# Optimization experiments

Hardware: AMD Instinct MI355X
Metric: run time of the kernel (lower is better)

## Reference

```python
import jax, jax.numpy as jnp
import numpy as np
from jax import lax

K = 3
PAD = 1
STRIDE = 1


def setup_inputs() -> dict:
    key = jax.random.key(0)
    k1, k2, k3 = jax.random.split(key, 3)
    B, Cin, Cout, H, W = 4, 64, 64, 128, 128
    x = jax.random.normal(k1, (B, Cin, H, W), dtype=jnp.float32)
    # offset-generating conv weight: [2*K*K, Cin, K, K]
    w_offset = jax.random.normal(k2, (2 * K * K, Cin, K, K), dtype=jnp.float32) * 0.05
    # deformable conv weight: [Cout, Cin, K, K]
    w_deform = jax.random.normal(k3, (Cout, Cin, K, K), dtype=jnp.float32) * 0.05
    return {"x": x, "w_offset": w_offset, "w_deform": w_deform}


def _bilinear_sample_one(img, ys, xs):
    # img: [C, H, W]; ys, xs: [K2, Ho, Wo] float sampling coords
    H, W = img.shape[1], img.shape[2]
    y0 = jnp.floor(ys)
    x0 = jnp.floor(xs)
    wy = ys - y0  # frac weights, [K2, Ho, Wo]
    wx = xs - x0

    def gather(yi, xi):
        valid = (yi >= 0) & (yi <= H - 1) & (xi >= 0) & (xi <= W - 1)
        yc = jnp.clip(yi, 0, H - 1).astype(jnp.int32)
        xc = jnp.clip(xi, 0, W - 1).astype(jnp.int32)
        # img[:, yc, xc] -> [C, K2, Ho, Wo]; zero outside (torchvision zero-pad)
        return img[:, yc, xc] * valid[None].astype(img.dtype)

    v00 = gather(y0, x0)
    v01 = gather(y0, x0 + 1)
    v10 = gather(y0 + 1, x0)
    v11 = gather(y0 + 1, x0 + 1)
    w00 = ((1 - wy) * (1 - wx))[None]
    w01 = ((1 - wy) * wx)[None]
    w10 = (wy * (1 - wx))[None]
    w11 = (wy * wx)[None]
    return v00 * w00 + v01 * w01 + v10 * w10 + v11 * w11  # [C, K2, Ho, Wo]


def reference(x, w_offset, w_deform):
    B, Cin, H, W = x.shape
    Cout = w_deform.shape[0]
    K2 = K * K
    # 1) plain conv to produce offsets: [B, 2*K2, H, W]
    offset = lax.conv_general_dilated(
        x, w_offset, window_strides=(STRIDE, STRIDE),
        padding=((PAD, PAD), (PAD, PAD)),
        dimension_numbers=("NCHW", "OIHW", "NCHW"))
    Ho, Wo = offset.shape[2], offset.shape[3]
    # torchvision ordering: channel 2*k = dy, 2*k+1 = dx, taps row-major
    off = offset.reshape(B, K2, 2, Ho, Wo)
    dy, dx = off[:, :, 0], off[:, :, 1]  # [B, K2, Ho, Wo]
    # 2) base sampling grid per kernel tap
    kk = jnp.arange(K2)
    ki = (kk // K).astype(jnp.float32)  # tap row
    kj = (kk % K).astype(jnp.float32)   # tap col
    base_y = (jnp.arange(Ho, dtype=jnp.float32) * STRIDE - PAD)[None, :] + ki[:, None]  # [K2, Ho]
    base_x = (jnp.arange(Wo, dtype=jnp.float32) * STRIDE - PAD)[None, :] + kj[:, None]  # [K2, Wo]
    ys = base_y[None, :, :, None] + dy  # [B, K2, Ho, Wo]
    xs = base_x[None, :, None, :] + dx
    # 3) deformable bilinear gather: [B, Cin, K2, Ho, Wo]
    sampled = jax.vmap(_bilinear_sample_one)(x, ys, xs)
    # 4) weighted accumulation (the conv contraction)
    out = jnp.einsum("ock,bckhw->bohw", w_deform.reshape(Cout, Cin, K2), sampled)
    return out
```

## Files before the change

### kernel.cpp

```cpp
#include <hip/hip_runtime.h>


#define BATCH 4
#define CIN   64
#define COUT  64
#define HH    128
#define WW    128
#define HWPIX (HH*WW)

typedef __attribute__((ext_vector_type(8))) short short8;
typedef __attribute__((ext_vector_type(4))) float floatx4;

__device__ __forceinline__ unsigned short f2bf(float f) {
  unsigned int u = __float_as_uint(f);
  unsigned int r = u + 0x7fffu + ((u >> 16) & 1u);
  return (unsigned short)(r >> 16);
}
__device__ __forceinline__ float bf2f(unsigned short h) { return __uint_as_float(((unsigned int)h) << 16); }
__device__ __forceinline__ float lo16f(unsigned int u) { return __uint_as_float(u << 16); }
__device__ __forceinline__ float hi16f(unsigned int u) { return __uint_as_float(u & 0xffff0000u); }

__device__ __forceinline__ unsigned int bilin2(unsigned int u00, unsigned int u01,
                                               unsigned int u10, unsigned int u11,
                                               float w00, float w01, float w10, float w11) {
  float lo = w00 * lo16f(u00) + w01 * lo16f(u01) + w10 * lo16f(u10) + w11 * lo16f(u11);
  float hi = w00 * hi16f(u00) + w01 * hi16f(u01) + w10 * hi16f(u10) + w11 * hi16f(u11);
  return (unsigned int)f2bf(lo) | ((unsigned int)f2bf(hi) << 16);
}

__global__ __launch_bounds__(256) void pre_kernel(const float* __restrict__ x,
                                                  const float* __restrict__ wo,
                                                  const float* __restrict__ wd,
                                                  unsigned short* __restrict__ xThi,
                                                  unsigned short* __restrict__ xTlo,
                                                  unsigned short* __restrict__ wdA,
                                                  unsigned short* __restrict__ woAhi,
                                                  unsigned short* __restrict__ woAlo) {
  int tid = threadIdx.x;
  if (blockIdx.x < 4096) {
    __shared__ float tile[32][33];
    int t = blockIdx.x;
    int b = t >> 10, rem = t & 1023;
    int c0 = (rem >> 9) * 32, p0 = (rem & 511) * 32;
    int tx = tid & 31, ty = tid >> 5;
    const float* xb = x + (size_t)b * CIN * HWPIX;
    size_t boff = (size_t)b * HWPIX * CIN;
#pragma unroll
    for (int i = 0; i < 4; i++)
      tile[ty + i * 8][tx] = xb[(size_t)(c0 + ty + i * 8) * HWPIX + p0 + tx];
    __syncthreads();
#pragma unroll
    for (int i = 0; i < 2; i++) {
      int tt = tid + i * 256;
      int row = tt >> 4;
      int cp = tt & 15;
      float v0 = tile[cp * 2][row], v1 = tile[cp * 2 + 1][row];
      unsigned short h0 = f2bf(v0), h1 = f2bf(v1);
      unsigned short l0 = f2bf(v0 - bf2f(h0)), l1 = f2bf(v1 - bf2f(h1));
      size_t o = boff + (size_t)(p0 + row) * CIN + c0 + cp * 2;
      *(ushort2*)&xThi[o] = make_ushort2(h0, h1);
      *(ushort2*)&xTlo[o] = make_ushort2(l0, l1);
    }
  } else {
    int t = (blockIdx.x - 4096) * 256 + tid;
    if (t < 36864) {
      int j = t & 7, lane = (t >> 3) & 63, ct = (t >> 9) & 3, kc = (t >> 11) & 1, kk = t >> 12;
      int cout = ct * 16 + (lane & 15);
      int cin  = kc * 32 + (lane >> 4) * 8 + j;
      wdA[t] = f2bf(wd[(size_t)(cout * CIN + cin) * 9 + kk]);
    }
    int t2 = t - 36864;
    if (t2 >= 0 && t2 < 18432) {
      int j = t2 & 7, lane = (t2 >> 3) & 63, ct = (t2 >> 9) & 1, kc = (t2 >> 10) & 1, kk = t2 >> 11;
      int cout = ct * 16 + (lane & 15);
      int cin  = kc * 32 + (lane >> 4) * 8 + j;
      float v = (cout < 18) ? wo[(size_t)(cout * CIN + cin) * 9 + kk] : 0.f;
      unsigned short h = f2bf(v);
      woAhi[t2] = h;
      woAlo[t2] = f2bf(v - bf2f(h));
    }
  }
}

__global__ __launch_bounds__(256) void fused_dcn_kernel(const unsigned short* __restrict__ xThi,
                                                        const unsigned short* __restrict__ xTlo,
                                                        const unsigned short* __restrict__ woAhi,
                                                        const unsigned short* __restrict__ woAlo,
                                                        const unsigned short* __restrict__ wdA,
                                                        float* __restrict__ out) {
  __shared__ unsigned short sBhi[4096];
  __shared__ unsigned short sBlo[4096];
  __shared__ float offL[18 * 64];

  int tid = threadIdx.x;
  int hw = blockIdx.x;
  int bid = (hw & 7) * 128 + (hw >> 3);
  int b = bid >> 8, r = bid & 255, y = r >> 1, x0 = (r & 1) << 6;

  int p1 = tid >> 2, si = tid & 3;
  int lane = tid & 63, w = tid >> 6;

  const unsigned short* xhib = xThi + (size_t)b * HWPIX * CIN;
  const unsigned short* xlob = xTlo + (size_t)b * HWPIX * CIN;

  int wq = p1 >> 4, iq = p1 & 15;
  int kcd = si >> 1, qb = si & 1;
  int dst0 = (((wq * 2 + kcd) * 64) + qb * 32 + iq) * 8;
  int dst1 = dst0 + 128;
  int xp = x0 + p1;

  floatx4 oacc[2];
  oacc[0] = (floatx4){0.f, 0.f, 0.f, 0.f};
  oacc[1] = (floatx4){0.f, 0.f, 0.f, 0.f};

#pragma unroll 1
  for (int kk = 0; kk < 9; kk++) {
    int ys = y - 1 + kk / 3;
    int xs = xp - 1 + kk % 3;
    bool valid = (ys >= 0) && (ys < HH) && (xs >= 0) && (xs < WW);
    uint4 h0 = {0, 0, 0, 0}, h1 = {0, 0, 0, 0}, l0 = {0, 0, 0, 0}, l1 = {0, 0, 0, 0};
    if (valid) {
      const unsigned short* ph = xhib + (size_t)(ys * WW + xs) * CIN + si * 16;
      const unsigned short* pl = xlob + (size_t)(ys * WW + xs) * CIN + si * 16;
      h0 = *(const uint4*)ph; h1 = *(const uint4*)(ph + 8);
      l0 = *(const uint4*)pl; l1 = *(const uint4*)(pl + 8);
    }
    *(uint4*)&sBhi[dst0] = h0; *(uint4*)&sBhi[dst1] = h1;
    *(uint4*)&sBlo[dst0] = l0; *(uint4*)&sBlo[dst1] = l1;
    __syncthreads();
    short8 bh0 = *(const short8*)&sBhi[(w * 2 + 0) * 512 + lane * 8];
    short8 bh1 = *(const short8*)&sBhi[(w * 2 + 1) * 512 + lane * 8];
    short8 bl0 = *(const short8*)&sBlo[(w * 2 + 0) * 512 + lane * 8];
    short8 bl1 = *(const short8*)&sBlo[(w * 2 + 1) * 512 + lane * 8];
    const short8* Ah = (const short8*)(woAhi + (size_t)kk * 2048);
    const short8* Al = (const short8*)(woAlo + (size_t)kk * 2048);
#pragma unroll
    for (int ct = 0; ct < 2; ct++) {
      short8 ah0 = Ah[ct * 64 + lane], ah1 = Ah[128 + ct * 64 + lane];
      short8 al0 = Al[ct * 64 + lane], al1 = Al[128 + ct * 64 + lane];
      oacc[ct] = __builtin_amdgcn_mfma_f32_16x16x32_bf16(ah0, bh0, oacc[ct], 0, 0, 0);
      oacc[ct] = __builtin_amdgcn_mfma_f32_16x16x32_bf16(ah0, bl0, oacc[ct], 0, 0, 0);
      oacc[ct] = __builtin_amdgcn_mfma_f32_16x16x32_bf16(al0, bh0, oacc[ct], 0, 0, 0);
      oacc[ct] = __builtin_amdgcn_mfma_f32_16x16x32_bf16(ah1, bh1, oacc[ct], 0, 0, 0);
      oacc[ct] = __builtin_amdgcn_mfma_f32_16x16x32_bf16(ah1, bl1, oacc[ct], 0, 0, 0);
      oacc[ct] = __builtin_amdgcn_mfma_f32_16x16x32_bf16(al1, bh1, oacc[ct], 0, 0, 0);
    }
    __syncthreads();
  }

  {
    int pxl = w * 16 + (lane & 15);
    int rowb = (lane >> 4) * 4;
#pragma unroll
    for (int ct = 0; ct < 2; ct++)
#pragma unroll
      for (int rr = 0; rr < 4; rr++) {
        int row = ct * 16 + rowb + rr;
        if (row < 18) offL[row * 64 + pxl] = oacc[ct][rr];
      }
  }
  __syncthreads();

  floatx4 acc[4];
#pragma unroll
  for (int ct = 0; ct < 4; ct++) acc[ct] = (floatx4){0.f, 0.f, 0.f, 0.f};

#pragma unroll 1
  for (int kk = 0; kk < 9; kk++) {
    {
      float dy = offL[(2 * kk) * 64 + p1];
      float dx = offL[(2 * kk + 1) * 64 + p1];
      float ys = (float)(y - 1 + kk / 3) + dy;
      float xs = (float)(xp - 1 + kk % 3) + dx;
      float y0f = floorf(ys), x0f = floorf(xs);
      float wy = ys - y0f, wx = xs - x0f;
      int iy0 = (int)y0f, ix0 = (int)x0f;
      int iy1 = iy0 + 1, ix1 = ix0 + 1;
      float w00 = (1.f - wy) * (1.f - wx), w01 = (1.f - wy) * wx;
      float w10 = wy * (1.f - wx), w11 = wy * wx;
      bool vy0 = (iy0 >= 0) && (iy0 < HH), vy1 = (iy1 >= 0) && (iy1 < HH);
      bool vx0 = (ix0 >= 0) && (ix0 < WW), vx1 = (ix1 >= 0) && (ix1 < WW);
      if (!(vy0 && vx0)) w00 = 0.f;
      if (!(vy0 && vx1)) w01 = 0.f;
      if (!(vy1 && vx0)) w10 = 0.f;
      if (!(vy1 && vx1)) w11 = 0.f;
      int cy0 = min(max(iy0, 0), HH - 1), cy1 = min(max(iy1, 0), HH - 1);
      int cx0 = min(max(ix0, 0), WW - 1), cx1 = min(max(ix1, 0), WW - 1);
      const unsigned short* q00 = xhib + (size_t)(cy0 * WW + cx0) * CIN + si * 16;
      const unsigned short* q01 = xhib + (size_t)(cy0 * WW + cx1) * CIN + si * 16;
      const unsigned short* q10 = xhib + (size_t)(cy1 * WW + cx0) * CIN + si * 16;
      const unsigned short* q11 = xhib + (size_t)(cy1 * WW + cx1) * CIN + si * 16;
      uint4 a00 = *(const uint4*)q00, a01 = *(const uint4*)q01;
      uint4 a10 = *(const uint4*)q10, a11 = *(const uint4*)q11;
      uint4 b00 = *(const uint4*)(q00 + 8), b01 = *(const uint4*)(q01 + 8);
      uint4 b10 = *(const uint4*)(q10 + 8), b11 = *(const uint4*)(q11 + 8);
      uint4 o0, o1;
      o0.x = bilin2(a00.x, a01.x, a10.x, a11.x, w00, w01, w10, w11);
      o0.y = bilin2(a00.y, a01.y, a10.y, a11.y, w00, w01, w10, w11);
      o0.z = bilin2(a00.z, a01.z, a10.z, a11.z, w00, w01, w10, w11);
      o0.w = bilin2(a00.w, a01.w, a10.w, a11.w, w00, w01, w10, w11);
      o1.x = bilin2(b00.x, b01.x, b10.x, b11.x, w00, w01, w10, w11);
      o1.y = bilin2(b00.y, b01.y, b10.y, b11.y, w00, w01, w10, w11);
      o1.z = bilin2(b00.z, b01.z, b10.z, b11.z, w00, w01, w10, w11);
      o1.w = bilin2(b00.w, b01.w, b10.w, b11.w, w00, w01, w10, w11);
      *(uint4*)&sBhi[dst0] = o0;
      *(uint4*)&sBhi[dst1] = o1;
    }
    __syncthreads();
    {
      short8 bv0 = *(const short8*)&sBhi[(w * 2 + 0) * 512 + lane * 8];
      short8 bv1 = *(const short8*)&sBhi[(w * 2 + 1) * 512 + lane * 8];
      const short8* Ap = (const short8*)(wdA + (size_t)kk * 4096);
#pragma unroll
      for (int ct = 0; ct < 4; ct++) {
        short8 a0 = Ap[ct * 64 + lane];
        short8 a1 = Ap[256 + ct * 64 + lane];
        acc[ct] = __builtin_amdgcn_mfma_f32_16x16x32_bf16(a0, bv0, acc[ct], 0, 0, 0);
        acc[ct] = __builtin_amdgcn_mfma_f32_16x16x32_bf16(a1, bv1, acc[ct], 0, 0, 0);
      }
    }
    __syncthreads();
  }

  int px = x0 + w * 16 + (lane & 15);
  int rowb = (lane >> 4) * 4;
  float* outb = out + (size_t)b * COUT * HWPIX + y * WW + px;
#pragma unroll
  for (int ct = 0; ct < 4; ct++)
#pragma unroll
    for (int rr = 0; rr < 4; rr++)
      outb[(size_t)(ct * 16 + rowb + rr) * HWPIX] = acc[ct][rr];
}

extern "C" void kernel_launch(void* const* d_in, const int* in_sizes, int n_in,
                              void* d_out, int out_size, void* d_ws, size_t ws_size,
                              hipStream_t stream) {
  const float* x  = (const float*)d_in[0];
  const float* wo = (const float*)d_in[1];
  const float* wd = (const float*)d_in[2];
  float* out = (float*)d_out;

  char* wsb = (char*)d_ws;
  unsigned short* xThi  = (unsigned short*)wsb;
  unsigned short* xTlo  = (unsigned short*)(wsb + 8388608);
  unsigned short* wdA   = (unsigned short*)(wsb + 16777216);
  unsigned short* woAhi = (unsigned short*)(wsb + 16777216 + 73728);
  unsigned short* woAlo = (unsigned short*)(wsb + 16850944 + 36864);

  pre_kernel<<<dim3(4096 + 216), dim3(256), 0, stream>>>(x, wo, wd, xThi, xTlo, wdA, woAhi, woAlo);
  fused_dcn_kernel<<<dim3(BATCH * HWPIX / 64), dim3(256), 0, stream>>>(xThi, xTlo, woAhi, woAlo, wdA, out);
}
```

Before: 114.6 us.

## Prefetch next tap's global loads into registers and swizzle LDS tiles

Both the offset-conv loop and the deformable-gather loop are software-pipelined. The global loads and the bilinear corner fetches for tap kk+1 are issued before tap kk's LDS store, barrier and MFMA work, so memory latency overlaps compute. Weight fragments are loaded before the barrier, LDS addresses get an XOR swizzle to cut bank conflicts, and a redundant barrier is dropped because each wave reads only the offsets it wrote itself. The cost is more live registers, since the prefetch buffer holds eight uint4 values plus weights, which could lower occupancy.

```diff
diff --git a/kernel.cpp b/kernel.cpp
--- a/kernel.cpp
+++ b/kernel.cpp
@@ -27,6 +27,8 @@
   float hi = w00 * hi16f(u00) + w01 * hi16f(u01) + w10 * hi16f(u10) + w11 * hi16f(u11);
   return (unsigned int)f2bf(lo) | ((unsigned int)f2bf(hi) << 16);
 }
+
+__device__ __forceinline__ int swz(int a) { return a ^ (((a >> 9) & 3) << 4); }
 
 __global__ __launch_bounds__(256) void pre_kernel(const float* __restrict__ x,
                                                   const float* __restrict__ wo,
@@ -105,47 +107,75 @@
 
   int wq = p1 >> 4, iq = p1 & 15;
   int kcd = si >> 1, qb = si & 1;
-  int dst0 = (((wq * 2 + kcd) * 64) + qb * 32 + iq) * 8;
-  int dst1 = dst0 + 128;
+  int wb0 = ((((wq * 2 + kcd) * 64) + qb * 32 + iq) * 8) * 2;
+  int wb1 = wb0 + 256;
+  unsigned short* stHi0 = (unsigned short*)((char*)sBhi + swz(wb0));
+  unsigned short* stHi1 = (unsigned short*)((char*)sBhi + swz(wb1));
+  unsigned short* stLo0 = (unsigned short*)((char*)sBlo + swz(wb0));
+  unsigned short* stLo1 = (unsigned short*)((char*)sBlo + swz(wb1));
+  int rb0 = (w * 2 + 0) * 1024 + lane * 16;
+  int rb1 = (w * 2 + 1) * 1024 + lane * 16;
+  const short8* rdHi0 = (const short8*)((const char*)sBhi + swz(rb0));
+  const short8* rdHi1 = (const short8*)((const char*)sBhi + swz(rb1));
+  const short8* rdLo0 = (const short8*)((const char*)sBlo + swz(rb0));
+  const short8* rdLo1 = (const short8*)((const char*)sBlo + swz(rb1));
+
   int xp = x0 + p1;
 
   floatx4 oacc[2];
   oacc[0] = (floatx4){0.f, 0.f, 0.f, 0.f};
   oacc[1] = (floatx4){0.f, 0.f, 0.f, 0.f};
 
-#pragma unroll 1
-  for (int kk = 0; kk < 9; kk++) {
+  auto ldA = [&](int kk, uint4& h0, uint4& h1, uint4& l0, uint4& l1) {
     int ys = y - 1 + kk / 3;
     int xs = xp - 1 + kk % 3;
     bool valid = (ys >= 0) && (ys < HH) && (xs >= 0) && (xs < WW);
-    uint4 h0 = {0, 0, 0, 0}, h1 = {0, 0, 0, 0}, l0 = {0, 0, 0, 0}, l1 = {0, 0, 0, 0};
+    h0 = (uint4){0, 0, 0, 0}; h1 = h0; l0 = h0; l1 = h0;
     if (valid) {
       const unsigned short* ph = xhib + (size_t)(ys * WW + xs) * CIN + si * 16;
       const unsigned short* pl = xlob + (size_t)(ys * WW + xs) * CIN + si * 16;
       h0 = *(const uint4*)ph; h1 = *(const uint4*)(ph + 8);
       l0 = *(const uint4*)pl; l1 = *(const uint4*)(pl + 8);
     }
-    *(uint4*)&sBhi[dst0] = h0; *(uint4*)&sBhi[dst1] = h1;
-    *(uint4*)&sBlo[dst0] = l0; *(uint4*)&sBlo[dst1] = l1;
-    __syncthreads();
-    short8 bh0 = *(const short8*)&sBhi[(w * 2 + 0) * 512 + lane * 8];
-    short8 bh1 = *(const short8*)&sBhi[(w * 2 + 1) * 512 + lane * 8];
-    short8 bl0 = *(const short8*)&sBlo[(w * 2 + 0) * 512 + lane * 8];
-    short8 bl1 = *(const short8*)&sBlo[(w * 2 + 1) * 512 + lane * 8];
+  };
+  auto bodyA = [&](int kk, const uint4& h0, const uint4& h1, const uint4& l0, const uint4& l1) {
     const short8* Ah = (const short8*)(woAhi + (size_t)kk * 2048);
     const short8* Al = (const short8*)(woAlo + (size_t)kk * 2048);
-#pragma unroll
-    for (int ct = 0; ct < 2; ct++) {
-      short8 ah0 = Ah[ct * 64 + lane], ah1 = Ah[128 + ct * 64 + lane];
-      short8 al0 = Al[ct * 64 + lane], al1 = Al[128 + ct * 64 + lane];
-      oacc[ct] = __builtin_amdgcn_mfma_f32_16x16x32_bf16(ah0, bh0, oacc[ct], 0, 0, 0);
-      oacc[ct] = __builtin_amdgcn_mfma_f32_16x16x32_bf16(ah0, bl0, oacc[ct], 0, 0, 0);
-      oacc[ct] = __builtin_amdgcn_mfma_f32_16x16x32_bf16(al0, bh0, oacc[ct], 0, 0, 0);
-      oacc[ct] = __builtin_amdgcn_mfma_f32_16x16x32_bf16(ah1, bh1, oacc[ct], 0, 0, 0);
-      oacc[ct] = __builtin_amdgcn_mfma_f32_16x16x32_bf16(ah1, bl1, oacc[ct], 0, 0, 0);
-      oacc[ct] = __builtin_amdgcn_mfma_f32_16x16x32_bf16(al1, bh1, oacc[ct], 0, 0, 0);
-    }
-    __syncthreads();
+    short8 ah0a = Ah[lane],       ah1a = Ah[128 + lane];
+    short8 al0a = Al[lane],       al1a = Al[128 + lane];
+    short8 ah0b = Ah[64 + lane],  ah1b = Ah[192 + lane];
+    short8 al0b = Al[64 + lane],  al1b = Al[192 + lane];
+    *(uint4*)stHi0 = h0; *(uint4*)stHi1 = h1;
+    *(uint4*)stLo0 = l0; *(uint4*)stLo1 = l1;
+    __syncthreads();
+    short8 bh0 = *rdHi0, bh1 = *rdHi1;
+    short8 bl0 = *rdLo0, bl1 = *rdLo1;
+    oacc[0] = __builtin_amdgcn_mfma_f32_16x16x32_bf16(ah0a, bh0, oacc[0], 0, 0, 0);
+    oacc[0] = __builtin_amdgcn_mfma_f32_16x16x32_bf16(ah0a, bl0, oacc[0], 0, 0, 0);
+    oacc[0] = __builtin_amdgcn_mfma_f32_16x16x32_bf16(al0a, bh0, oacc[0], 0, 0, 0);
+    oacc[0] = __builtin_amdgcn_mfma_f32_16x16x32_bf16(ah1a, bh1, oacc[0], 0, 0, 0);
+    oacc[0] = __builtin_amdgcn_mfma_f32_16x16x32_bf16(ah1a, bl1, oacc[0], 0, 0, 0);
+    oacc[0] = __builtin_amdgcn_mfma_f32_16x16x32_bf16(al1a, bh1, oacc[0], 0, 0, 0);
+    oacc[1] = __builtin_amdgcn_mfma_f32_16x16x32_bf16(ah0b, bh0, oacc[1], 0, 0, 0);
+    oacc[1] = __builtin_amdgcn_mfma_f32_16x16x32_bf16(ah0b, bl0, oacc[1], 0, 0, 0);
+    oacc[1] = __builtin_amdgcn_mfma_f32_16x16x32_bf16(al0b, bh0, oacc[1], 0, 0, 0);
+    oacc[1] = __builtin_amdgcn_mfma_f32_16x16x32_bf16(ah1b, bh1, oacc[1], 0, 0, 0);
+    oacc[1] = __builtin_amdgcn_mfma_f32_16x16x32_bf16(ah1b, bl1, oacc[1], 0, 0, 0);
+    oacc[1] = __builtin_amdgcn_mfma_f32_16x16x32_bf16(al1b, bh1, oacc[1], 0, 0, 0);
+    __syncthreads();
+  };
+
+  {
+    uint4 h0c, h1c, l0c, l1c;
+    ldA(0, h0c, h1c, l0c, l1c);
+#pragma unroll 1
+    for (int kk = 0; kk < 8; kk++) {
+      uint4 h0n, h1n, l0n, l1n;
+      ldA(kk + 1, h0n, h1n, l0n, l1n);
+      bodyA(kk, h0c, h1c, l0c, l1c);
+      h0c = h0n; h1c = h1n; l0c = l0n; l1c = l1n;
+    }
+    bodyA(8, h0c, h1c, l0c, l1c);
   }
 
   {
@@ -159,67 +189,84 @@
         if (row < 18) offL[row * 64 + pxl] = oacc[ct][rr];
       }
   }
-  __syncthreads();
 
   floatx4 acc[4];
 #pragma unroll
   for (int ct = 0; ct < 4; ct++) acc[ct] = (floatx4){0.f, 0.f, 0.f, 0.f};
 
+  struct BS {
+    float w00, w01, w10, w11;
+    uint4 a00, a01, a10, a11, b00, b01, b10, b11;
+  };
+  auto ldB = [&](int kk) -> BS {
+    BS s;
+    float dy = offL[(2 * kk) * 64 + p1];
+    float dx = offL[(2 * kk + 1) * 64 + p1];
+    float ys = (float)(y - 1 + kk / 3) + dy;
+    float xs = (float)(xp - 1 + kk % 3) + dx;
+    float y0f = floorf(ys), x0f = floorf(xs);
+    float wy = ys - y0f, wx = xs - x0f;
+    int iy0 = (int)y0f, ix0 = (int)x0f;
+    int iy1 = iy0 + 1, ix1 = ix0 + 1;
+    s.w00 = (1.f - wy) * (1.f - wx); s.w01 = (1.f - wy) * wx;
+    s.w10 = wy * (1.f - wx);         s.w11 = wy * wx;
+    bool vy0 = (iy0 >= 0) && (iy0 < HH), vy1 = (iy1 >= 0) && (iy1 < HH);
+    bool vx0 = (ix0 >= 0) && (ix0 < WW), vx1 = (ix1 >= 0) && (ix1 < WW);
+    if (!(vy0 && vx0)) s.w00 = 0.f;
+    if (!(vy0 && vx1)) s.w01 = 0.f;
+    if (!(vy1 && vx0)) s.w10 = 0.f;
+    if (!(vy1 && vx1)) s.w11 = 0.f;
+    int cy0 = min(max(iy0, 0), HH - 1), cy1 = min(max(iy1, 0), HH - 1);
+    int cx0 = min(max(ix0, 0), WW - 1), cx1 = min(max(ix1, 0), WW - 1);
+    const unsigned short* q00 = xhib + (size_t)(cy0 * WW + cx0) * CIN + si * 16;
+    const unsigned short* q01 = xhib + (size_t)(cy0 * WW + cx1) * CIN + si * 16;
+    const unsigned short* q10 = xhib + (size_t)(cy1 * WW + cx0) * CIN + si * 16;
+    const unsigned short* q11 = xhib + (size_t)(cy1 * WW + cx1) * CIN + si * 16;
+    s.a00 = *(const uint4*)q00; s.a01 = *(const uint4*)q01;
+    s.a10 = *(const uint4*)q10; s.a11 = *(const uint4*)q11;
+    s.b00 = *(const uint4*)(q00 + 8); s.b01 = *(const uint4*)(q01 + 8);
+    s.b10 = *(const uint4*)(q10 + 8); s.b11 = *(const uint4*)(q11 + 8);
+    return s;
+  };
+  auto bodyB = [&](int kk, const BS& s) {
+    const short8* Ap = (const short8*)(wdA + (size_t)kk * 4096);
+    short8 a0q0 = Ap[lane],        a1q0 = Ap[256 + lane];
+    short8 a0q1 = Ap[64 + lane],   a1q1 = Ap[320 + lane];
+    short8 a0q2 = Ap[128 + lane],  a1q2 = Ap[384 + lane];
+    short8 a0q3 = Ap[192 + lane],  a1q3 = Ap[448 + lane];
+    uint4 o0, o1;
+    o0.x = bilin2(s.a00.x, s.a01.x, s.a10.x, s.a11.x, s.w00, s.w01, s.w10, s.w11);
+    o0.y = bilin2(s.a00.y, s.a01.y, s.a10.y, s.a11.y, s.w00, s.w01, s.w10, s.w11);
+    o0.z = bilin2(s.a00.z, s.a01.z, s.a10.z, s.a11.z, s.w00, s.w01, s.w10, s.w11);
+    o0.w = bilin2(s.a00.w, s.a01.w, s.a10.w, s.a11.w, s.w00, s.w01, s.w10, s.w11);
+    o1.x = bilin2(s.b00.x, s.b01.x, s.b10.x, s.b11.x, s.w00, s.w01, s.w10, s.w11);
+    o1.y = bilin2(s.b00.y, s.b01.y, s.b10.y, s.b11.y, s.w00, s.w01, s.w10, s.w11);
+    o1.z = bilin2(s.b00.z, s.b01.z, s.b10.z, s.b11.z, s.w00, s.w01, s.w10, s.w11);
+    o1.w = bilin2(s.b00.w, s.b01.w, s.b10.w, s.b11.w, s.w00, s.w01, s.w10, s.w11);
+    *(uint4*)stHi0 = o0;
+    *(uint4*)stHi1 = o1;
+    __syncthreads();
+    short8 bv0 = *rdHi0, bv1 = *rdHi1;
+    acc[0] = __builtin_amdgcn_mfma_f32_16x16x32_bf16(a0q0, bv0, acc[0], 0, 0, 0);
+    acc[0] = __builtin_amdgcn_mfma_f32_16x16x32_bf16(a1q0, bv1, acc[0], 0, 0, 0);
+    acc[1] = __builtin_amdgcn_mfma_f32_16x16x32_bf16(a0q1, bv0, acc[1], 0, 0, 0);
+    acc[1] = __builtin_amdgcn_mfma_f32_16x16x32_bf16(a1q1, bv1, acc[1], 0, 0, 0);
+    acc[2] = __builtin_amdgcn_mfma_f32_16x16x32_bf16(a0q2, bv0, acc[2], 0, 0, 0);
+    acc[2] = __builtin_amdgcn_mfma_f32_16x16x32_bf16(a1q2, bv1, acc[2], 0, 0, 0);
+    acc[3] = __builtin_amdgcn_mfma_f32_16x16x32_bf16(a0q3, bv0, acc[3], 0, 0, 0);
+    acc[3] = __builtin_amdgcn_mfma_f32_16x16x32_bf16(a1q3, bv1, acc[3], 0, 0, 0);
+    __syncthreads();
+  };
+
+  {
+    BS sc = ldB(0);
 #pragma unroll 1
-  for (int kk = 0; kk < 9; kk++) {
-    {
-      float dy = offL[(2 * kk) * 64 + p1];
-      float dx = offL[(2 * kk + 1) * 64 + p1];
-      float ys = (float)(y - 1 + kk / 3) + dy;
-      float xs = (float)(xp - 1 + kk % 3) + dx;
-      float y0f = floorf(ys), x0f = floorf(xs);
-      float wy = ys - y0f, wx = xs - x0f;
-      int iy0 = (int)y0f, ix0 = (int)x0f;
-      int iy1 = iy0 + 1, ix1 = ix0 + 1;
-      float w00 = (1.f - wy) * (1.f - wx), w01 = (1.f - wy) * wx;
-      float w10 = wy * (1.f - wx), w11 = wy * wx;
-      bool vy0 = (iy0 >= 0) && (iy0 < HH), vy1 = (iy1 >= 0) && (iy1 < HH);
-      bool vx0 = (ix0 >= 0) && (ix0 < WW), vx1 = (ix1 >= 0) && (ix1 < WW);
-      if (!(vy0 && vx0)) w00 = 0.f;
-      if (!(vy0 && vx1)) w01 = 0.f;
-      if (!(vy1 && vx0)) w10 = 0.f;
-      if (!(vy1 && vx1)) w11 = 0.f;
-      int cy0 = min(max(iy0, 0), HH - 1), cy1 = min(max(iy1, 0), HH - 1);
-      int cx0 = min(max(ix0, 0), WW - 1), cx1 = min(max(ix1, 0), WW - 1);
-      const unsigned short* q00 = xhib + (size_t)(cy0 * WW + cx0) * CIN + si * 16;
-      const unsigned short* q01 = xhib + (size_t)(cy0 * WW + cx1) * CIN + si * 16;
-      const unsigned short* q10 = xhib + (size_t)(cy1 * WW + cx0) * CIN + si * 16;
-      const unsigned short* q11 = xhib + (size_t)(cy1 * WW + cx1) * CIN + si * 16;
-      uint4 a00 = *(const uint4*)q00, a01 = *(const uint4*)q01;
-      uint4 a10 = *(const uint4*)q10, a11 = *(const uint4*)q11;
-      uint4 b00 = *(const uint4*)(q00 + 8), b01 = *(const uint4*)(q01 + 8);
-      uint4 b10 = *(const uint4*)(q10 + 8), b11 = *(const uint4*)(q11 + 8);
-      uint4 o0, o1;
-      o0.x = bilin2(a00.x, a01.x, a10.x, a11.x, w00, w01, w10, w11);
-      o0.y = bilin2(a00.y, a01.y, a10.y, a11.y, w00, w01, w10, w11);
-      o0.z = bilin2(a00.z, a01.z, a10.z, a11.z, w00, w01, w10, w11);
-      o0.w = bilin2(a00.w, a01.w, a10.w, a11.w, w00, w01, w10, w11);
-      o1.x = bilin2(b00.x, b01.x, b10.x, b11.x, w00, w01, w10, w11);
-      o1.y = bilin2(b00.y, b01.y, b10.y, b11.y, w00, w01, w10, w11);
-      o1.z = bilin2(b00.z, b01.z, b10.z, b11.z, w00, w01, w10, w11);
-      o1.w = bilin2(b00.w, b01.w, b10.w, b11.w, w00, w01, w10, w11);
-      *(uint4*)&sBhi[dst0] = o0;
-      *(uint4*)&sBhi[dst1] = o1;
-    }
-    __syncthreads();
-    {
-      short8 bv0 = *(const short8*)&sBhi[(w * 2 + 0) * 512 + lane * 8];
-      short8 bv1 = *(const short8*)&sBhi[(w * 2 + 1) * 512 + lane * 8];
-      const short8* Ap = (const short8*)(wdA + (size_t)kk * 4096);
-#pragma unroll
-      for (int ct = 0; ct < 4; ct++) {
-        short8 a0 = Ap[ct * 64 + lane];
-        short8 a1 = Ap[256 + ct * 64 + lane];
-        acc[ct] = __builtin_amdgcn_mfma_f32_16x16x32_bf16(a0, bv0, acc[ct], 0, 0, 0);
-        acc[ct] = __builtin_amdgcn_mfma_f32_16x16x32_bf16(a1, bv1, acc[ct], 0, 0, 0);
-      }
-    }
-    __syncthreads();
+    for (int kk = 0; kk < 8; kk++) {
+      BS sn = ldB(kk + 1);
+      bodyB(kk, sc);
+      sc = sn;
+    }
+    bodyB(8, sc);
   }
 
   int px = x0 + w * 16 + (lane & 15);
```

New measurement: 115.5 us. No clear change (+0.8%).

## Halve pixels per block, split Cin across wave groups, swizzle LDS

Applied to the files above, without the earlier changes.

Each block now handles 32 pixels instead of 64, and the grid doubles to 2048 blocks. In the deformable phase the four waves are split into two groups that each handle half of Cin, and the partial sums are reduced through LDS before the store. Each thread gathers 8 channels instead of 16, and hi/lo are staged in one XOR-swizzled LDS buffer to avoid bank conflicts. The aim is more parallelism and shorter per-thread gather latency, at the cost of an extra LDS reduction, a sync, and idle waves in the offset-conv phase.

```diff
diff --git a/kernel.cpp b/kernel.cpp
--- a/kernel.cpp
+++ b/kernel.cpp
@@ -27,6 +27,8 @@
   float hi = w00 * hi16f(u00) + w01 * hi16f(u01) + w10 * hi16f(u10) + w11 * hi16f(u11);
   return (unsigned int)f2bf(lo) | ((unsigned int)f2bf(hi) << 16);
 }
+
+__device__ __forceinline__ int swzB(int a) { return a ^ (((a >> 8) & 7) << 4); }
 
 __global__ __launch_bounds__(256) void pre_kernel(const float* __restrict__ x,
                                                   const float* __restrict__ wo,
@@ -88,52 +90,51 @@
                                                         const unsigned short* __restrict__ woAlo,
                                                         const unsigned short* __restrict__ wdA,
                                                         float* __restrict__ out) {
-  __shared__ unsigned short sBhi[4096];
-  __shared__ unsigned short sBlo[4096];
-  __shared__ float offL[18 * 64];
+  __shared__ unsigned short sB[4096];
+  __shared__ float offL[18 * 32];
+  char* sBc = (char*)sB;
 
   int tid = threadIdx.x;
   int hw = blockIdx.x;
-  int bid = (hw & 7) * 128 + (hw >> 3);
-  int b = bid >> 8, r = bid & 255, y = r >> 1, x0 = (r & 1) << 6;
-
-  int p1 = tid >> 2, si = tid & 3;
+  int bid = (hw & 7) * 256 + (hw >> 3);
+  int b = bid >> 9, r = bid & 511, y = r >> 2, x0 = (r & 3) << 5;
+
   int lane = tid & 63, w = tid >> 6;
+  int wv = w & 1, wg = w >> 1;
+  int p1 = tid >> 3, o = tid & 7;
+  int xp = x0 + p1;
 
   const unsigned short* xhib = xThi + (size_t)b * HWPIX * CIN;
   const unsigned short* xlob = xTlo + (size_t)b * HWPIX * CIN;
-
-  int wq = p1 >> 4, iq = p1 & 15;
-  int kcd = si >> 1, qb = si & 1;
-  int dst0 = (((wq * 2 + kcd) * 64) + qb * 32 + iq) * 8;
-  int dst1 = dst0 + 128;
-  int xp = x0 + p1;
 
   floatx4 oacc[2];
   oacc[0] = (floatx4){0.f, 0.f, 0.f, 0.f};
   oacc[1] = (floatx4){0.f, 0.f, 0.f, 0.f};
+
+  int siA = o & 3;
+  int abase = ((o < 4) ? 0 : 4096) +
+              (((p1 >> 4) * 2 + (siA >> 1)) << 10) + ((siA & 1) << 9) + ((p1 & 15) << 4);
 
 #pragma unroll 1
   for (int kk = 0; kk < 9; kk++) {
     int ys = y - 1 + kk / 3;
     int xs = xp - 1 + kk % 3;
     bool valid = (ys >= 0) && (ys < HH) && (xs >= 0) && (xs < WW);
-    uint4 h0 = {0, 0, 0, 0}, h1 = {0, 0, 0, 0}, l0 = {0, 0, 0, 0}, l1 = {0, 0, 0, 0};
+    uint4 v0 = {0, 0, 0, 0}, v1 = {0, 0, 0, 0};
     if (valid) {
-      const unsigned short* ph = xhib + (size_t)(ys * WW + xs) * CIN + si * 16;
-      const unsigned short* pl = xlob + (size_t)(ys * WW + xs) * CIN + si * 16;
-      h0 = *(const uint4*)ph; h1 = *(const uint4*)(ph + 8);
-      l0 = *(const uint4*)pl; l1 = *(const uint4*)(pl + 8);
-    }
-    *(uint4*)&sBhi[dst0] = h0; *(uint4*)&sBhi[dst1] = h1;
-    *(uint4*)&sBlo[dst0] = l0; *(uint4*)&sBlo[dst1] = l1;
-    __syncthreads();
-    short8 bh0 = *(const short8*)&sBhi[(w * 2 + 0) * 512 + lane * 8];
-    short8 bh1 = *(const short8*)&sBhi[(w * 2 + 1) * 512 + lane * 8];
-    short8 bl0 = *(const short8*)&sBlo[(w * 2 + 0) * 512 + lane * 8];
-    short8 bl1 = *(const short8*)&sBlo[(w * 2 + 1) * 512 + lane * 8];
+      const unsigned short* arr = (o < 4) ? xhib : xlob;
+      const unsigned short* ph = arr + (size_t)(ys * WW + xs) * CIN + siA * 16;
+      v0 = *(const uint4*)ph; v1 = *(const uint4*)(ph + 8);
+    }
+    *(uint4*)(sBc + swzB(abase)) = v0;
+    *(uint4*)(sBc + swzB(abase + 256)) = v1;
+    __syncthreads();
     const short8* Ah = (const short8*)(woAhi + (size_t)kk * 2048);
     const short8* Al = (const short8*)(woAlo + (size_t)kk * 2048);
+    short8 bh0 = *(const short8*)(sBc + swzB(wv * 2048 + lane * 16));
+    short8 bh1 = *(const short8*)(sBc + swzB(wv * 2048 + 1024 + lane * 16));
+    short8 bl0 = *(const short8*)(sBc + swzB(4096 + wv * 2048 + lane * 16));
+    short8 bl1 = *(const short8*)(sBc + swzB(4096 + wv * 2048 + 1024 + lane * 16));
 #pragma unroll
     for (int ct = 0; ct < 2; ct++) {
       short8 ah0 = Ah[ct * 64 + lane], ah1 = Ah[128 + ct * 64 + lane];
@@ -148,15 +149,15 @@
     __syncthreads();
   }
 
-  {
-    int pxl = w * 16 + (lane & 15);
+  if (wg == 0) {
+    int wcol = wv * 16 + (lane & 15);
     int rowb = (lane >> 4) * 4;
 #pragma unroll
     for (int ct = 0; ct < 2; ct++)
 #pragma unroll
       for (int rr = 0; rr < 4; rr++) {
         int row = ct * 16 + rowb + rr;
-        if (row < 18) offL[row * 64 + pxl] = oacc[ct][rr];
+        if (row < 18) offL[row * 32 + wcol] = oacc[ct][rr];
       }
   }
   __syncthreads();
@@ -164,12 +165,15 @@
   floatx4 acc[4];
 #pragma unroll
   for (int ct = 0; ct < 4; ct++) acc[ct] = (floatx4){0.f, 0.f, 0.f, 0.f};
+
+  int bbase = (((p1 >> 4) * 2 + (o >> 2)) << 10) + ((o & 3) << 8) + ((p1 & 15) << 4);
+  int rdB = wv * 2048 + wg * 1024 + lane * 16;
 
 #pragma unroll 1
   for (int kk = 0; kk < 9; kk++) {
     {
-      float dy = offL[(2 * kk) * 64 + p1];
-      float dx = offL[(2 * kk + 1) * 64 + p1];
+      float dy = offL[(2 * kk) * 32 + p1];
+      float dx = offL[(2 * kk + 1) * 32 + p1];
       float ys = (float)(y - 1 + kk / 3) + dy;
       float xs = (float)(xp - 1 + kk % 3) + dx;
       float y0f = floorf(ys), x0f = floorf(xs);
@@ -186,50 +190,51 @@
       if (!(vy1 && vx1)) w11 = 0.f;
       int cy0 = min(max(iy0, 0), HH - 1), cy1 = min(max(iy1, 0), HH - 1);
       int cx0 = min(max(ix0, 0), WW - 1), cx1 = min(max(ix1, 0), WW - 1);
-      const unsigned short* q00 = xhib + (size_t)(cy0 * WW + cx0) * CIN + si * 16;
-      const unsigned short* q01 = xhib + (size_t)(cy0 * WW + cx1) * CIN + si * 16;
-      const unsigned short* q10 = xhib + (size_t)(cy1 * WW + cx0) * CIN + si * 16;
-      const unsigned short* q11 = xhib + (size_t)(cy1 * WW + cx1) * CIN + si * 16;
+      const unsigned short* q00 = xhib + (size_t)(cy0 * WW + cx0) * CIN + o * 8;
+      const unsigned short* q01 = xhib + (size_t)(cy0 * WW + cx1) * CIN + o * 8;
+      const unsigned short* q10 = xhib + (size_t)(cy1 * WW + cx0) * CIN + o * 8;
+      const unsigned short* q11 = xhib + (size_t)(cy1 * WW + cx1) * CIN + o * 8;
       uint4 a00 = *(const uint4*)q00, a01 = *(const uint4*)q01;
       uint4 a10 = *(const uint4*)q10, a11 = *(const uint4*)q11;
-      uint4 b00 = *(const uint4*)(q00 + 8), b01 = *(const uint4*)(q01 + 8);
-      uint4 b10 = *(const uint4*)(q10 + 8), b11 = *(const uint4*)(q11 + 8);
-      uint4 o0, o1;
+      uint4 o0;
       o0.x = bilin2(a00.x, a01.x, a10.x, a11.x, w00, w01, w10, w11);
       o0.y = bilin2(a00.y, a01.y, a10.y, a11.y, w00, w01, w10, w11);
       o0.z = bilin2(a00.z, a01.z, a10.z, a11.z, w00, w01, w10, w11);
       o0.w = bilin2(a00.w, a01.w, a10.w, a11.w, w00, w01, w10, w11);
-      o1.x = bilin2(b00.x, b01.x, b10.x, b11.x, w00, w01, w10, w11);
-      o1.y = bilin2(b00.y, b01.y, b10.y, b11.y, w00, w01, w10, w11);
-      o1.z = bilin2(b00.z, b01.z, b10.z, b11.z, w00, w01, w10, w11);
-      o1.w = bilin2(b00.w, b01.w, b10.w, b11.w, w00, w01, w10, w11);
-      *(uint4*)&sBhi[dst0] = o0;
-      *(uint4*)&sBhi[dst1] = o1;
+      *(uint4*)(sBc + swzB(bbase)) = o0;
     }
     __syncthreads();
     {
-      short8 bv0 = *(const short8*)&sBhi[(w * 2 + 0) * 512 + lane * 8];
-      short8 bv1 = *(const short8*)&sBhi[(w * 2 + 1) * 512 + lane * 8];
-      const short8* Ap = (const short8*)(wdA + (size_t)kk * 4096);
+      short8 bv = *(const short8*)(sBc + swzB(rdB));
+      const unsigned short* Ap = wdA + (size_t)kk * 4096 + wg * 2048;
 #pragma unroll
       for (int ct = 0; ct < 4; ct++) {
-        short8 a0 = Ap[ct * 64 + lane];
-        short8 a1 = Ap[256 + ct * 64 + lane];
-        acc[ct] = __builtin_amdgcn_mfma_f32_16x16x32_bf16(a0, bv0, acc[ct], 0, 0, 0);
-        acc[ct] = __builtin_amdgcn_mfma_f32_16x16x32_bf16(a1, bv1, acc[ct], 0, 0, 0);
+        short8 a = *(const short8*)(Ap + ct * 512 + lane * 8);
+        acc[ct] = __builtin_amdgcn_mfma_f32_16x16x32_bf16(a, bv, acc[ct], 0, 0, 0);
       }
     }
     __syncthreads();
   }
 
-  int px = x0 + w * 16 + (lane & 15);
-  int rowb = (lane >> 4) * 4;
-  float* outb = out + (size_t)b * COUT * HWPIX + y * WW + px;
-#pragma unroll
-  for (int ct = 0; ct < 4; ct++)
-#pragma unroll
-    for (int rr = 0; rr < 4; rr++)
-      outb[(size_t)(ct * 16 + rowb + rr) * HWPIX] = acc[ct][rr];
+  float* rf = (float*)sB;
+  if (wg == 1) {
+#pragma unroll
+    for (int ct = 0; ct < 4; ct++)
+      *(floatx4*)&rf[(((ct * 2) + wv) * 64 + lane) * 4] = acc[ct];
+  }
+  __syncthreads();
+  if (wg == 0) {
+    int px = x0 + wv * 16 + (lane & 15);
+    int rowb = (lane >> 4) * 4;
+    float* outb = out + (size_t)b * COUT * HWPIX + y * WW + px;
+#pragma unroll
+    for (int ct = 0; ct < 4; ct++) {
+      floatx4 other = *(floatx4*)&rf[(((ct * 2) + wv) * 64 + lane) * 4];
+#pragma unroll
+      for (int rr = 0; rr < 4; rr++)
+        outb[(size_t)(ct * 16 + rowb + rr) * HWPIX] = acc[ct][rr] + other[rr];
+    }
+  }
 }
 
 extern "C" void kernel_launch(void* const* d_in, const int* in_sizes, int n_in,
@@ -248,5 +253,5 @@
   unsigned short* woAlo = (unsigned short*)(wsb + 16850944 + 36864);
 
   pre_kernel<<<dim3(4096 + 216), dim3(256), 0, stream>>>(x, wo, wd, xThi, xTlo, wdA, woAhi, woAlo);
-  fused_dcn_kernel<<<dim3(BATCH * HWPIX / 64), dim3(256), 0, stream>>>(xThi, xTlo, woAhi, woAlo, wdA, out);
-}
+  fused_dcn_kernel<<<dim3(2048), dim3(256), 0, stream>>>(xThi, xTlo, woAhi, woAlo, wdA, out);
+}
```

Measured after the change: 125.5 us. 9.5% more time.
